# Kernel tuning notes

Measured on AMD Instinct MI355X. Metric: run time of the kernel, lower is better.

The kernel has to match this reference:

```python
import jax, jax.numpy as jnp
import numpy as np


def _apply_ring(x, angles):
    """Apply x @ R^T where R = G_0 @ G_1 @ ... @ G_{n-1} with ring planes
    (k, (k+1) % n). Equivalent to applying G_k^T to x for k = n-1 .. 0:
      x[:, k] <- c*x[:, k] - s*x[:, j]
      x[:, j] <- s*x[:, k] + c*x[:, j]
    x: [B, n], angles: [n].
    """
    n = angles.shape[0]

    def step(xT, k):
        a = angles[k]
        c, s = jnp.cos(a), jnp.sin(a)
        j = jnp.mod(k + 1, n)
        xi = xT[k]
        xj = xT[j]
        xT = xT.at[k].set(c * xi - s * xj)
        xT = xT.at[j].set(s * xi + c * xj)
        return xT, None

    ks = jnp.arange(n - 1, -1, -1)  # reverse order: R^T = G_{n-1}^T ... G_0^T
    xT, _ = jax.lax.scan(step, x.T, ks)  # carry is [n, B]
    return xT.T


def setup_inputs() -> dict:
    key = jax.random.key(0)
    k_x, k_e, k_d = jax.random.split(key, 3)
    B, n, num_blocks = 8192, 1024, 4
    return {
        "x": jax.random.normal(k_x, (B, n), dtype=jnp.float32),
        "angles_enc": jax.random.normal(k_e, (num_blocks, n), dtype=jnp.float32),
        "angles_dec": jax.random.normal(k_d, (num_blocks, n), dtype=jnp.float32),
        "hidden_weight": jnp.zeros((1,), dtype=jnp.float32),
        "hidden_state": jnp.zeros((n,), dtype=jnp.float32),
    }


def reference(x, angles_enc, angles_dec, hidden_weight, hidden_state):
    num_blocks = angles_enc.shape[0]
    b = x
    for blk in range(num_blocks):
        b = _apply_ring(b, angles_enc[blk])
    # recurrent blend; weight uses the detached hidden_weight (original uses
    # numpy on .detach()), so stop_gradient matches the original semantics.
    w = jax.nn.sigmoid(jax.lax.stop_gradient(hidden_weight[0]))
    bottleneck = (1.0 - w) * b + w * hidden_state[None, :]
    out = bottleneck
    for blk in range(num_blocks):
        out = _apply_ring(out, angles_dec[blk])
    return (bottleneck, out)
```

## Files before the change

kernel.cpp:

```cpp
#include <hip/hip_runtime.h>
#include <math.h>

#define N_COLS 1024
#define NRINGS 8

#define TPR    64
#define CHUNK  16
#define ROWS_PER_BLOCK 8

#define F_OFF   16384
#define A_OFF   24576
#define AUX_OFF 25088
#define WS_FLOATS 25104

typedef const __attribute__((address_space(1))) float4* gas_f4;
typedef __attribute__((address_space(3))) void* las_ptr;

__global__ __launch_bounds__(256)
void ced_setup(const float* __restrict__ ae,
               const float* __restrict__ ad,
               float* __restrict__ ws)
{
    __shared__ float2 ls[256];
    const int r   = blockIdx.x >> 2;
    const int b   = blockIdx.x & 3;
    const int tid = threadIdx.x;
    const int k   = (b << 8) + tid;
    const float* ang = (r < 4) ? (ae + (r << 10)) : (ad + ((r - 4) << 10));

    float sv, cv;
    sincosf(ang[k], &sv, &cv);
    if (k == N_COLS - 1) {
        ((float2*)(ws + AUX_OFF))[r] = make_float2(cv, sv);
        cv = 0.f; sv = -1.f;
    }
    ls[tid] = make_float2(cv, sv);
    __syncthreads();

    if (!(tid & 1)) {
        float2 e0 = ls[tid], e1 = ls[tid + 1];
        int t  = k >> 4;
        int jp = (k & 15) >> 1;
        ((float4*)ws)[(r*8 + jp)*64 + t] = make_float4(e0.x, e0.y, e1.x, e1.y);
    }

    if (tid < 64) {
        const int lt = tid >> 2;
        const int q  = tid & 3;
        const int t  = (b << 4) + lt;
        const int j0 = lt * CHUNK + 4 * q;
        float2 e0 = ls[j0], e1 = ls[j0+1], e2 = ls[j0+2], e3 = ls[j0+3];

        float f3 = e3.x;       float P = -e3.y;
        float f2 = e2.x * P;   P *= -e2.y;
        float f1 = e1.x * P;   P *= -e1.y;
        float f0 = e0.x * P;   P *= -e0.y;

        float ip = P;
        #pragma unroll
        for (int d = 1; d < 4; d <<= 1) {
            float tmp = __shfl_down(ip, d);
            if (q + d < 4) ip *= tmp;
        }
        float ex = __shfl_down(ip, 1);
        if (q == 3) ex = 1.f;
        f0 *= ex; f1 *= ex; f2 *= ex; f3 *= ex;

        ((float4*)(ws + F_OFF))[(r*4 + q)*64 + t] = make_float4(f0, f1, f2, f3);
        if (q == 0) ws[A_OFF + r*TPR + t] = ip;
    }
}

__global__ __launch_bounds__(512, 4)
void ced_main(const float* __restrict__ x,
              const float* __restrict__ ws,
              const float* __restrict__ hw,
              const float* __restrict__ hs,
              float* __restrict__ out, int B)
{
    __shared__ float4 sCS[2][512];
    __shared__ float4 sF [2][256];
    __shared__ float4 sA4[128];
    __shared__ float4 sAux4[4];

    const float4* CSg = (const float4*)ws;
    const float4* Fg  = (const float4*)(ws + F_OFF);

    const int tid = threadIdx.x;
    const int t   = tid & 63;
    const int row = blockIdx.x * ROWS_PER_BLOCK + (tid >> 6);
    const size_t rowOff = (size_t)row * N_COLS;

    __builtin_amdgcn_global_load_lds((gas_f4)(CSg + tid),
                                     (las_ptr)&sCS[0][tid], 16, 0, 0);
    if (tid < 256)
        __builtin_amdgcn_global_load_lds((gas_f4)(Fg + tid),
                                         (las_ptr)&sF[0][tid], 16, 0, 0);

    if (tid < 128)                sA4[tid]         = ((const float4*)(ws + A_OFF))[tid];
    if (tid >= 128 && tid < 132)  sAux4[tid - 128] = ((const float4*)(ws + AUX_OFF))[tid - 128];

    float y[CHUNK];
    {
        const float4* xp = (const float4*)(x + rowOff + t * CHUNK);
        #pragma unroll
        for (int i = 0; i < 4; ++i) {
            float4 v = xp[i];
            y[4*i] = v.x; y[4*i+1] = v.y; y[4*i+2] = v.z; y[4*i+3] = v.w;
        }
    }

    const float w   = 1.f / (1.f + expf(-hw[0]));
    const float omw = 1.f - w;

    __syncthreads();

    const float*  As   = (const float*)sA4;
    const float2* Auxs = (const float2*)sAux4;

    #pragma unroll 1
    for (int r = 0; r < NRINGS; ++r) {
        if (r < NRINGS - 1) {
            const int nb = (r + 1) & 1;
            __builtin_amdgcn_global_load_lds((gas_f4)(CSg + (r + 1) * 512 + tid),
                                             (las_ptr)&sCS[nb][tid], 16, 0, 0);
            if (tid < 256)
                __builtin_amdgcn_global_load_lds((gas_f4)(Fg + (r + 1) * 256 + tid),
                                                 (las_ptr)&sF[nb][tid], 16, 0, 0);
        }

        if (r == 4) {
            float4* oa = (float4*)(out + rowOff + t * CHUNK);
            const float4* hp = (const float4*)(hs + t * CHUNK);
            #pragma unroll
            for (int i = 0; i < 4; ++i) {
                float4 h = hp[i];
                float4 nb2;
                nb2.x = fmaf(omw, y[4*i+0], w * h.x);
                nb2.y = fmaf(omw, y[4*i+1], w * h.y);
                nb2.z = fmaf(omw, y[4*i+2], w * h.z);
                nb2.w = fmaf(omw, y[4*i+3], w * h.w);
                oa[i] = nb2;
                y[4*i+0] = nb2.x; y[4*i+1] = nb2.y; y[4*i+2] = nb2.z; y[4*i+3] = nb2.w;
            }
        }

        const int buf = r & 1;
        const float4* csL = &sCS[buf][0];
        const float4* fL  = &sF [buf][0];
        const float2  cN  = Auxs[r];
        const float   saI = As[r * TPR + t];

        float y0 = __shfl(y[0],       0);
        float yN = __shfl(y[CHUNK-1], 63);
        float Cinit = cN.x * yN - cN.y * y0;
        float x0n   = fmaf(cN.y, yN, cN.x * y0);
        if (t == 0) y[0] = x0n;

        float car = 0.f, zt = 0.f;
        #pragma unroll
        for (int jp = CHUNK/2 - 1; jp >= 0; --jp) {
            float4 cs4 = csL[jp * 64 + t];
            const int j1 = 2*jp + 1;
            float z1 = fmaf(cs4.w, y[j1], cs4.z * car);
            car = fmaf(-cs4.w, car, cs4.z * y[j1]);
            if (j1 == CHUNK - 1) zt = z1;
            else                 y[j1+1] = z1;
            const int j0 = 2*jp;
            float z0 = fmaf(cs4.y, y[j0], cs4.x * car);
            car = fmaf(-cs4.y, car, cs4.x * y[j0]);
            y[j0+1] = z0;
        }

        float sa = saI, sb = car;
        #pragma unroll
        for (int d = 1; d < TPR; d <<= 1) {
            float a2 = __shfl_down(sa, d);
            float b2 = __shfl_down(sb, d);
            if (t + d < TPR) { sb = fmaf(sa, b2, sb); sa *= a2; }
        }
        float ea = __shfl_down(sa, 1);
        float eb = __shfl_down(sb, 1);
        float zf  = fmaf(sa, Cinit, sb);
        float Cin = (t == TPR - 1) ? Cinit : fmaf(ea, Cinit, eb);

        #pragma unroll
        for (int qi = CHUNK/4 - 1; qi >= 0; --qi) {
            float4 f4 = fL[qi * 64 + t];
            const int j = 4*qi;
            if (j + 3 == CHUNK - 1) zt = fmaf(f4.w, Cin, zt);
            else                    y[j+4] = fmaf(f4.w, Cin, y[j+4]);
            y[j+3] = fmaf(f4.z, Cin, y[j+3]);
            y[j+2] = fmaf(f4.y, Cin, y[j+2]);
            y[j+1] = fmaf(f4.x, Cin, y[j+1]);
        }

        float up = __shfl_up(zt, 1);
        y[0] = (t == 0) ? zf : up;

        if (r < NRINGS - 1) __syncthreads();
    }

    float4* oo = (float4*)(out + (size_t)B * N_COLS + rowOff + t * CHUNK);
    #pragma unroll
    for (int i = 0; i < 4; ++i)
        oo[i] = make_float4(y[4*i], y[4*i+1], y[4*i+2], y[4*i+3]);
}

__global__ __launch_bounds__(256, 2)
void ced_fallback(const float* __restrict__ x,
                  const float* __restrict__ ae,
                  const float* __restrict__ ad,
                  const float* __restrict__ hw,
                  const float* __restrict__ hs,
                  float* __restrict__ out, int B)
{
    __shared__ float2 s_cs[NRINGS * 64 * 16];
    __shared__ float  s_A [NRINGS * 16];
    __shared__ float2 s_aux[NRINGS];

    const int tid = threadIdx.x;
    for (int i = 0; i < 32; ++i) {
        int idx = i * 256 + tid;
        int r   = idx >> 10;
        int k   = idx & 1023;
        const float* ang = (r < 4) ? (ae + (r << 10)) : (ad + ((r - 4) << 10));
        float sv, cv;
        sincosf(ang[k], &sv, &cv);
        int t = k >> 6, j = k & 63;
        float2 e = make_float2(cv, sv);
        if (k == 1023) { s_aux[r] = e; e = make_float2(0.f, -1.f); }
        s_cs[(r * 64 + j) * 16 + t] = e;
    }
    __syncthreads();
    if (tid < NRINGS * 16) {
        int r = tid >> 4, t = tid & 15;
        float p = 1.f;
        for (int j = 0; j < 64; ++j) p *= -s_cs[(r * 64 + j) * 16 + t].y;
        s_A[tid] = p;
    }
    __syncthreads();

    const int lane      = tid & 63;
    const int g         = lane >> 4;
    const int t         = lane & 15;
    const int groupBase = lane & 48;
    const int row       = blockIdx.x * 16 + (tid >> 6) * 4 + g;

    const float* xr = x + (size_t)row * N_COLS + t * 64;
    float y[64];
    #pragma unroll
    for (int i = 0; i < 16; ++i) {
        float4 v = ((const float4*)xr)[i];
        y[4*i] = v.x; y[4*i+1] = v.y; y[4*i+2] = v.z; y[4*i+3] = v.w;
    }
    const float w   = 1.f / (1.f + expf(-hw[0]));
    const float omw = 1.f - w;

    for (int r = 0; r < NRINGS; ++r) {
        if (r == 4) {
            float4* ob = (float4*)(out + (size_t)row * N_COLS + t * 64);
            const float4* hp = (const float4*)(hs + t * 64);
            #pragma unroll
            for (int i = 0; i < 16; ++i) {
                float4 h = hp[i];
                float4 bn;
                bn.x = fmaf(omw, y[4*i+0], w * h.x);
                bn.y = fmaf(omw, y[4*i+1], w * h.y);
                bn.z = fmaf(omw, y[4*i+2], w * h.z);
                bn.w = fmaf(omw, y[4*i+3], w * h.w);
                ob[i] = bn;
                y[4*i+0] = bn.x; y[4*i+1] = bn.y; y[4*i+2] = bn.z; y[4*i+3] = bn.w;
            }
        }
        const float2* csr = s_cs + r * 64 * 16;
        const float2  cN  = s_aux[r];
        float y0 = __shfl(y[0],  groupBase);
        float yN = __shfl(y[63], groupBase + 15);
        float Cinit = cN.x * yN - cN.y * y0;
        float x0n   = fmaf(cN.y, yN, cN.x * y0);
        if (t == 0) y[0] = x0n;

        float carry = 0.f, ztmp = 0.f;
        #pragma unroll
        for (int j = 63; j >= 0; --j) {
            float2 cs = csr[j * 16 + t];
            float z   = fmaf(cs.y, y[j], cs.x * carry);
            carry     = fmaf(-cs.y, carry, cs.x * y[j]);
            if (j == 63) ztmp = z; else y[j + 1] = z;
        }
        float sa = s_A[r * 16 + t], sb = carry;
        #pragma unroll
        for (int d = 1; d < 16; d <<= 1) {
            float a2 = __shfl_down(sa, d);
            float b2 = __shfl_down(sb, d);
            if (t + d < 16) { sb = fmaf(sa, b2, sb); sa *= a2; }
        }
        float ea = __shfl_down(sa, 1);
        float eb = __shfl_down(sb, 1);
        float z0  = fmaf(sa, Cinit, sb);
        float Cin = (t == 15) ? Cinit : fmaf(ea, Cinit, eb);

        float P = 1.f;
        #pragma unroll
        for (int j = 63; j >= 0; --j) {
            float2 cs = csr[j * 16 + t];
            float f = cs.x * P;
            P = -cs.y * P;
            if (j == 63) ztmp = fmaf(f, Cin, ztmp);
            else         y[j + 1] = fmaf(f, Cin, y[j + 1]);
        }
        float up = __shfl_up(ztmp, 1);
        y[0] = (t == 0) ? z0 : up;
    }

    float4* oo = (float4*)(out + (size_t)B * N_COLS + (size_t)row * N_COLS + t * 64);
    #pragma unroll
    for (int i = 0; i < 16; ++i)
        oo[i] = make_float4(y[4*i], y[4*i+1], y[4*i+2], y[4*i+3]);
}

extern "C" void kernel_launch(void* const* d_in, const int* in_sizes, int n_in,
                              void* d_out, int out_size, void* d_ws, size_t ws_size,
                              hipStream_t stream) {
    const float* x  = (const float*)d_in[0];
    const float* ae = (const float*)d_in[1];
    const float* ad = (const float*)d_in[2];
    const float* hw = (const float*)d_in[3];
    const float* hs = (const float*)d_in[4];
    float* out = (float*)d_out;
    const int B = in_sizes[0] / N_COLS;

    if (ws_size >= WS_FLOATS * sizeof(float) && (B % ROWS_PER_BLOCK) == 0) {
        hipLaunchKernelGGL(ced_setup, dim3(32), dim3(256), 0, stream,
                           ae, ad, (float*)d_ws);
        hipLaunchKernelGGL(ced_main, dim3(B / ROWS_PER_BLOCK), dim3(512), 0, stream,
                           x, (const float*)d_ws, hw, hs, out, B);
    } else {
        hipLaunchKernelGGL(ced_fallback, dim3(B / 16), dim3(256), 0, stream,
                           x, ae, ad, hw, hs, out, B);
    }
}
```

Baseline: 129.3 us.

## Read ring coefficients directly from global memory instead of LDS staging

```diff
diff --git a/kernel.cpp b/kernel.cpp
--- a/kernel.cpp
+++ b/kernel.cpp
@@ -6,15 +6,12 @@
 
 #define TPR    64
 #define CHUNK  16
-#define ROWS_PER_BLOCK 8
-
-#define F_OFF   16384
-#define A_OFF   24576
-#define AUX_OFF 25088
+#define ROWS_PER_BLOCK 4
+
+#define F_OFF    16384
+#define A_OFF    24576
+#define AUX_OFF  25088
 #define WS_FLOATS 25104
-
-typedef const __attribute__((address_space(1))) float4* gas_f4;
-typedef __attribute__((address_space(3))) void* las_ptr;
 
 __global__ __launch_bounds__(256)
 void ced_setup(const float* __restrict__ ae,
@@ -71,34 +68,22 @@
     }
 }
 
-__global__ __launch_bounds__(512, 4)
+__global__ __launch_bounds__(256, 4)
 void ced_main(const float* __restrict__ x,
               const float* __restrict__ ws,
               const float* __restrict__ hw,
               const float* __restrict__ hs,
               float* __restrict__ out, int B)
 {
-    __shared__ float4 sCS[2][512];
-    __shared__ float4 sF [2][256];
-    __shared__ float4 sA4[128];
-    __shared__ float4 sAux4[4];
-
-    const float4* CSg = (const float4*)ws;
-    const float4* Fg  = (const float4*)(ws + F_OFF);
-
     const int tid = threadIdx.x;
     const int t   = tid & 63;
     const int row = blockIdx.x * ROWS_PER_BLOCK + (tid >> 6);
     const size_t rowOff = (size_t)row * N_COLS;
 
-    __builtin_amdgcn_global_load_lds((gas_f4)(CSg + tid),
-                                     (las_ptr)&sCS[0][tid], 16, 0, 0);
-    if (tid < 256)
-        __builtin_amdgcn_global_load_lds((gas_f4)(Fg + tid),
-                                         (las_ptr)&sF[0][tid], 16, 0, 0);
-
-    if (tid < 128)                sA4[tid]         = ((const float4*)(ws + A_OFF))[tid];
-    if (tid >= 128 && tid < 132)  sAux4[tid - 128] = ((const float4*)(ws + AUX_OFF))[tid - 128];
+    const float4* CSg  = (const float4*)ws;
+    const float4* Fg   = (const float4*)(ws + F_OFF);
+    const float*  Ag   = ws + A_OFF;
+    const float2* AUXg = (const float2*)(ws + AUX_OFF);
 
     float y[CHUNK];
     {
@@ -113,22 +98,8 @@
     const float w   = 1.f / (1.f + expf(-hw[0]));
     const float omw = 1.f - w;
 
-    __syncthreads();
-
-    const float*  As   = (const float*)sA4;
-    const float2* Auxs = (const float2*)sAux4;
-
     #pragma unroll 1
     for (int r = 0; r < NRINGS; ++r) {
-        if (r < NRINGS - 1) {
-            const int nb = (r + 1) & 1;
-            __builtin_amdgcn_global_load_lds((gas_f4)(CSg + (r + 1) * 512 + tid),
-                                             (las_ptr)&sCS[nb][tid], 16, 0, 0);
-            if (tid < 256)
-                __builtin_amdgcn_global_load_lds((gas_f4)(Fg + (r + 1) * 256 + tid),
-                                                 (las_ptr)&sF[nb][tid], 16, 0, 0);
-        }
-
         if (r == 4) {
             float4* oa = (float4*)(out + rowOff + t * CHUNK);
             const float4* hp = (const float4*)(hs + t * CHUNK);
@@ -145,11 +116,10 @@
             }
         }
 
-        const int buf = r & 1;
-        const float4* csL = &sCS[buf][0];
-        const float4* fL  = &sF [buf][0];
-        const float2  cN  = Auxs[r];
-        const float   saI = As[r * TPR + t];
+        const float4* cs = CSg + r * 512;
+        const float4* fp = Fg  + r * 256;
+        const float2  cN  = AUXg[r];
+        const float   saI = Ag[r * TPR + t];
 
         float y0 = __shfl(y[0],       0);
         float yN = __shfl(y[CHUNK-1], 63);
@@ -160,7 +130,7 @@
         float car = 0.f, zt = 0.f;
         #pragma unroll
         for (int jp = CHUNK/2 - 1; jp >= 0; --jp) {
-            float4 cs4 = csL[jp * 64 + t];
+            float4 cs4 = cs[jp * 64 + t];
             const int j1 = 2*jp + 1;
             float z1 = fmaf(cs4.w, y[j1], cs4.z * car);
             car = fmaf(-cs4.w, car, cs4.z * y[j1]);
@@ -186,7 +156,7 @@
 
         #pragma unroll
         for (int qi = CHUNK/4 - 1; qi >= 0; --qi) {
-            float4 f4 = fL[qi * 64 + t];
+            float4 f4 = fp[qi * 64 + t];
             const int j = 4*qi;
             if (j + 3 == CHUNK - 1) zt = fmaf(f4.w, Cin, zt);
             else                    y[j+4] = fmaf(f4.w, Cin, y[j+4]);
@@ -197,8 +167,6 @@
 
         float up = __shfl_up(zt, 1);
         y[0] = (t == 0) ? zf : up;
-
-        if (r < NRINGS - 1) __syncthreads();
     }
 
     float4* oo = (float4*)(out + (size_t)B * N_COLS + rowOff + t * CHUNK);
@@ -334,7 +302,7 @@
     if (ws_size >= WS_FLOATS * sizeof(float) && (B % ROWS_PER_BLOCK) == 0) {
         hipLaunchKernelGGL(ced_setup, dim3(32), dim3(256), 0, stream,
                            ae, ad, (float*)d_ws);
-        hipLaunchKernelGGL(ced_main, dim3(B / ROWS_PER_BLOCK), dim3(512), 0, stream,
+        hipLaunchKernelGGL(ced_main, dim3(B / ROWS_PER_BLOCK), dim3(256), 0, stream,
                            x, (const float*)d_ws, hw, hs, out, B);
     } else {
         hipLaunchKernelGGL(ced_fallback, dim3(B / 16), dim3(256), 0, stream,
```

Result: no change. 130.0 us (+0.5%).
